# Kernel tuning notes

Hardware: AMD Instinct MI355X
Metric: run time of the kernel (lower is better)

## Reference

```python
import jax, jax.numpy as jnp
import numpy as np

HID = 2048      # hidden_size
H = 16          # num_heads == num_kv_heads (stack in fwd forces MHA)
DH = HID // H   # head_size = 128
QKV = 3 * H * DH  # 6144
THETA = 10000.0
EPS = 1e-5      # flash-attn RMSNorm default eps
B, L = 4, 2048


def setup_inputs() -> dict:
    key = jax.random.key(0)
    k1, k2, k3 = jax.random.split(key, 3)
    hidden_states = jax.random.normal(k1, (B, L, HID), dtype=jnp.float32)
    # weights stored as (in, out); scaled like a typical init so activations stay sane
    W_qkvg = jax.random.normal(k2, (HID, QKV + HID), dtype=jnp.float32) * 0.02
    W_out = jax.random.normal(k3, (HID, HID), dtype=jnp.float32) * 0.02
    return {"hidden_states": hidden_states, "W_qkvg": W_qkvg, "W_out": W_out}


def _rmsnorm(x):
    # elementwise_affine=False: pure rms normalization over head dim
    return x * jax.lax.rsqrt(jnp.mean(x * x, axis=-1, keepdims=True) + EPS)


def _rope(x, seqlen_offset=0):
    # x: (B, L, H, DH), non-interleaved (GPT-NeoX style rotate-half)
    half = DH // 2
    inv_freq = 1.0 / (THETA ** (jnp.arange(half, dtype=jnp.float32) * 2.0 / DH))
    pos = jnp.arange(seqlen_offset, seqlen_offset + x.shape[1], dtype=jnp.float32)
    ang = pos[:, None] * inv_freq[None, :]                  # (L, half)
    cos = jnp.cos(ang)[None, :, None, :]                    # (1,L,1,half)
    sin = jnp.sin(ang)[None, :, None, :]
    x1, x2 = x[..., :half], x[..., half:]
    return jnp.concatenate([x1 * cos - x2 * sin, x1 * sin + x2 * cos], axis=-1)


def _attention_forward(hidden_states, W_qkvg, W_out):
    b, l, _ = hidden_states.shape
    proj = hidden_states @ W_qkvg                           # (B,L,QKV+HID)
    qkv_flat, gate = proj[..., :QKV], proj[..., QKV:]
    gate = jax.nn.sigmoid(gate)
    qkv = qkv_flat.reshape(b, l, 3 * H, DH)
    q, k, v = qkv[:, :, :H], qkv[:, :, H:2 * H], qkv[:, :, 2 * H:]
    q = _rope(_rmsnorm(q))
    k = _rope(_rmsnorm(k))
    # causal softmax attention (math of flash_attn_func)
    scores = jnp.einsum('blhd,bmhd->bhlm', q, k) / np.sqrt(DH).astype(np.float32)
    causal = jnp.tril(jnp.ones((l, l), dtype=bool))
    scores = jnp.where(causal[None, None], scores, jnp.finfo(scores.dtype).min)
    attn = jax.nn.softmax(scores, axis=-1)
    out = jnp.einsum('bhlm,bmhd->blhd', attn, v).reshape(b, l, HID)
    out = out * gate
    return out @ W_out


def reference(hidden_states, W_qkvg, W_out):
    return _attention_forward(hidden_states, W_qkvg, W_out)
```

## Files before the change

### kernel.cpp

```cpp
#include <hip/hip_runtime.h>


typedef __attribute__((ext_vector_type(8))) short bf16x8;
typedef __attribute__((ext_vector_type(4))) float f32x4;
typedef __attribute__((ext_vector_type(4))) unsigned short us4;

#if __has_builtin(__builtin_amdgcn_exp2f)
#define EXP2(x) __builtin_amdgcn_exp2f(x)
#else
#define EXP2(x) exp2f(x)
#endif

__device__ __forceinline__ unsigned short f2bf(float f) {
    unsigned int x = __float_as_uint(f);
    unsigned int r = x + 0x7fffu + ((x >> 16) & 1u);
    return (unsigned short)(r >> 16);
}
__device__ __forceinline__ unsigned short f2bf_fast(float f) {
    return (unsigned short)((__float_as_uint(f) + 0x8000u) >> 16);
}
__device__ __forceinline__ float bf2f(unsigned short u) {
    return __uint_as_float(((unsigned int)u) << 16);
}

__device__ __forceinline__ void gll16(const unsigned short* g, unsigned short* l) {
    __builtin_amdgcn_global_load_lds(
        (const __attribute__((address_space(1))) unsigned int*)g,
        (__attribute__((address_space(3))) unsigned int*)l, 16, 0, 0);
}

__global__ __launch_bounds__(256) void cvt_bf16(const float* __restrict__ in,
                                                unsigned short* __restrict__ out) {
    int i = blockIdx.x * 256 + threadIdx.x;
    float4 v = ((const float4*)in)[i];
    us4 r;
    r[0] = f2bf(v.x); r[1] = f2bf(v.y); r[2] = f2bf(v.z); r[3] = f2bf(v.w);
    ((us4*)out)[i] = r;
}

__global__ __launch_bounds__(256) void transpose_cvt(const float* __restrict__ in,
                                                     unsigned short* __restrict__ out,
                                                     int R, int C) {
    __shared__ float t[32][33];
    int c0 = blockIdx.x * 32, r0 = blockIdx.y * 32;
    int tx = threadIdx.x, ty = threadIdx.y;
#pragma unroll
    for (int i = 0; i < 4; i++)
        t[ty + i * 8][tx] = in[(size_t)(r0 + ty + i * 8) * C + c0 + tx];
    __syncthreads();
#pragma unroll
    for (int i = 0; i < 4; i++)
        out[(size_t)(c0 + ty + i * 8) * R + r0 + tx] = f2bf(t[tx][ty + i * 8]);
}

__device__ __forceinline__ void gemm_core(const unsigned short* __restrict__ A,
                                          const unsigned short* __restrict__ Bt,
                                          int K, int rowA0, int colB0,
                                          unsigned short* As, unsigned short* Bs,
                                          f32x4 acc[4][4]) {
    const int tid = threadIdx.x;
    const int w = tid >> 6, lane = tid & 63;
    const int quad = lane >> 4, l15 = lane & 15;
    const int wm = w >> 1, wn = w & 1;
    const int lr = lane >> 3;
    const int lc = ((lane & 7) ^ lr) * 8;

    const unsigned short* ga[4]; const unsigned short* gb[4];
    unsigned short* la[4]; unsigned short* lb[4];
#pragma unroll
    for (int i = 0; i < 4; i++) {
        int r = w * 32 + i * 8;
        ga[i] = A  + (size_t)(rowA0 + r + lr) * K + lc;
        gb[i] = Bt + (size_t)(colB0 + r + lr) * K + lc;
        la[i] = As + r * 64;
        lb[i] = Bs + r * 64;
    }
    const int sw = (l15 & 7);
    const int KT = K >> 6;
    for (int kt = 0; kt < KT; kt++) {
        const int ko = kt * 64;
#pragma unroll
        for (int i = 0; i < 4; i++) gll16(ga[i] + ko, la[i]);
#pragma unroll
        for (int i = 0; i < 4; i++) gll16(gb[i] + ko, lb[i]);
        __syncthreads();
#pragma unroll
        for (int kk = 0; kk < 2; kk++) {
            bf16x8 af[4], bfr[4];
#pragma unroll
            for (int mi = 0; mi < 4; mi++)
                af[mi] = *(const bf16x8*)&As[(wm * 64 + mi * 16 + l15) * 64 +
                                             (((kk * 4 + quad) ^ sw) * 8)];
#pragma unroll
            for (int ni = 0; ni < 4; ni++)
                bfr[ni] = *(const bf16x8*)&Bs[(wn * 64 + ni * 16 + l15) * 64 +
                                              (((kk * 4 + quad) ^ sw) * 8)];
#pragma unroll
            for (int mi = 0; mi < 4; mi++)
#pragma unroll
                for (int ni = 0; ni < 4; ni++)
                    acc[mi][ni] = __builtin_amdgcn_mfma_f32_16x16x32_bf16(
                        af[mi], bfr[ni], acc[mi][ni], 0, 0, 0);
        }
        __syncthreads();
    }
}

__global__ __launch_bounds__(256) void gemm_qkvg(const unsigned short* __restrict__ A,
                                                 const unsigned short* __restrict__ Bt,
                                                 unsigned short* __restrict__ Qb,
                                                 unsigned short* __restrict__ Kb,
                                                 unsigned short* __restrict__ Vt,
                                                 unsigned short* __restrict__ Gb) {
    __shared__ unsigned short smem[128 * 128];
    unsigned short* As = smem;
    unsigned short* Bs = smem + 128 * 64;
    f32x4 acc[4][4];
    f32x4 z = {0.f, 0.f, 0.f, 0.f};
#pragma unroll
    for (int i = 0; i < 4; i++)
#pragma unroll
        for (int j = 0; j < 4; j++) acc[i][j] = z;

    const int rowA0 = blockIdx.y * 128, colB0 = blockIdx.x * 128;
    gemm_core(A, Bt, 2048, rowA0, colB0, As, Bs, acc);

    const int tid = threadIdx.x, w = tid >> 6, lane = tid & 63;
    const int quad = lane >> 4, l15 = lane & 15;
    const int wm = w >> 1, wn = w & 1;
    const int sec = blockIdx.x >> 4;
    const int h = blockIdx.x & 15;

    if (sec == 2) {
        __syncthreads();
#pragma unroll
        for (int mi = 0; mi < 4; mi++)
#pragma unroll
            for (int ni = 0; ni < 4; ni++)
#pragma unroll
                for (int i = 0; i < 4; i++) {
                    int ll = wm * 64 + mi * 16 + quad * 4 + i;
                    int d  = wn * 64 + ni * 16 + l15;
                    smem[d * 128 + (((ll >> 3) ^ (d & 15)) * 8) + (ll & 7)] =
                        f2bf(acc[mi][ni][i]);
                }
        __syncthreads();
        const int b_ = rowA0 >> 11, l0 = rowA0 & 2047;
        const int r = tid >> 1, hf = tid & 1;
        unsigned short* drow = Vt + (size_t)(b_ * 16 + h) * 128 * 2048 +
                               (size_t)r * 2048 + l0;
#pragma unroll
        for (int jj = 0; jj < 8; jj++) {
            int jcol = hf * 8 + jj;
            *(bf16x8*)(drow + jcol * 8) =
                *(const bf16x8*)&smem[r * 128 + ((jcol ^ (r & 15)) * 8)];
        }
    } else if (sec == 3) {
#pragma unroll
        for (int mi = 0; mi < 4; mi++)
#pragma unroll
            for (int ni = 0; ni < 4; ni++)
#pragma unroll
                for (int i = 0; i < 4; i++) {
                    int rowg = rowA0 + wm * 64 + mi * 16 + quad * 4 + i;
                    int d = wn * 64 + ni * 16 + l15;
                    float g = 1.f / (1.f + __expf(-acc[mi][ni][i]));
                    Gb[((size_t)rowg << 11) + h * 128 + d] = f2bf(g);
                }
    } else {
        unsigned short* dst = (sec == 0) ? Qb : Kb;
#pragma unroll
        for (int mi = 0; mi < 4; mi++)
#pragma unroll
            for (int ni = 0; ni < 4; ni++)
#pragma unroll
                for (int i = 0; i < 4; i++) {
                    int rowg = rowA0 + wm * 64 + mi * 16 + quad * 4 + i;
                    int d = wn * 64 + ni * 16 + l15;
                    int b_ = rowg >> 11, l_ = rowg & 2047;
                    dst[(((size_t)(b_ * 16 + h) * 2048 + l_) << 7) + d] =
                        f2bf(acc[mi][ni][i]);
                }
    }
}

__global__ __launch_bounds__(256) void gemm_out(const unsigned short* __restrict__ A,
                                                const unsigned short* __restrict__ Bt,
                                                float* __restrict__ C) {
    __shared__ unsigned short As[128 * 64], Bs[128 * 64];
    f32x4 acc[4][4];
    f32x4 z = {0.f, 0.f, 0.f, 0.f};
#pragma unroll
    for (int i = 0; i < 4; i++)
#pragma unroll
        for (int j = 0; j < 4; j++) acc[i][j] = z;

    const int rowA0 = blockIdx.y * 128, colB0 = blockIdx.x * 128;
    gemm_core(A, Bt, 2048, rowA0, colB0, As, Bs, acc);

    const int tid = threadIdx.x, w = tid >> 6, lane = tid & 63;
    const int quad = lane >> 4, l15 = lane & 15;
    const int wm = w >> 1, wn = w & 1;
#pragma unroll
    for (int mi = 0; mi < 4; mi++)
#pragma unroll
        for (int ni = 0; ni < 4; ni++)
#pragma unroll
            for (int i = 0; i < 4; i++) {
                int rowg = rowA0 + wm * 64 + mi * 16 + quad * 4 + i;
                int col = colB0 + wn * 64 + ni * 16 + l15;
                C[(size_t)rowg * 2048 + col] = acc[mi][ni][i];
            }
}

__global__ __launch_bounds__(256) void rmsnorm_rope(unsigned short* __restrict__ Qp,
                                                    unsigned short* __restrict__ Kp) {
    unsigned short* X = blockIdx.y ? Kp : Qp;
    const int tid = threadIdx.x;
    const int row = blockIdx.x * 4 + (tid >> 6);
    const int lane = tid & 63;
    unsigned short* p = X + (size_t)row * 128;
    const int l_ = row & 2047;
    float x1 = bf2f(p[lane]);
    float x2 = bf2f(p[lane + 64]);
    float ss = x1 * x1 + x2 * x2;
#pragma unroll
    for (int off = 32; off >= 1; off >>= 1) ss += __shfl_xor(ss, off, 64);
    float r = rsqrtf(ss * (1.f / 128.f) + 1e-5f);
    x1 *= r; x2 *= r;
    float inv = exp2f(-(float)lane * (13.287712379549449f / 64.f));
    float ang = (float)l_ * inv;
    float sn, cs;
    sincosf(ang, &sn, &cs);
    p[lane]      = f2bf(x1 * cs - x2 * sn);
    p[lane + 64] = f2bf(x1 * sn + x2 * cs);
}

__global__ __launch_bounds__(512) void fa_kernel(const unsigned short* __restrict__ Q,
                                                 const unsigned short* __restrict__ K,
                                                 const unsigned short* __restrict__ Vt,
                                                 const unsigned short* __restrict__ G,
                                                 unsigned short* __restrict__ Og) {
    __shared__ unsigned short Ks[64 * 128];
    __shared__ unsigned short Vs[128 * 64];
    __shared__ unsigned short Ps[256 * 32];
    const int g = blockIdx.x;
    const int bh = (g & 7) | ((g >> 6) << 3);
    const int qc = (g >> 3) & 7;
    const int tid = threadIdx.x, w = tid >> 6, lane = tid & 63;
    const int quad = lane >> 4, l15 = lane & 15;
    const int sw = l15 & 7;
    const int qrow0 = qc * 256 + w * 32;
    const float CS = 0.12751740395609812f;

    bf16x8 qf[2][4];
#pragma unroll
    for (int mi = 0; mi < 2; mi++)
#pragma unroll
        for (int kt = 0; kt < 4; kt++)
            qf[mi][kt] = *(const bf16x8*)(Q + ((size_t)bh * 2048 + qrow0 + mi * 16 + l15) * 128
                                             + kt * 32 + quad * 8);

    f32x4 o[2][8];
    f32x4 z = {0.f, 0.f, 0.f, 0.f};
#pragma unroll
    for (int mi = 0; mi < 2; mi++)
#pragma unroll
        for (int nj = 0; nj < 8; nj++) o[mi][nj] = z;
    float rowsum[2][4];
#pragma unroll
    for (int mi = 0; mi < 2; mi++)
#pragma unroll
        for (int i = 0; i < 4; i++) rowsum[mi][i] = 0.f;

    const unsigned short* Kbase = K + (size_t)bh * 2048 * 128;
    const unsigned short* Vtb   = Vt + (size_t)bh * 128 * 2048;

    const int pr0 = w * 32 + l15, pr1 = pr0 + 16;
    const int pk0 = (pr0 >> 1) & 3, pk1 = (pr1 >> 1) & 3;

    const int NJ = 4 * (qc + 1);
    for (int j = 0; j < NJ; j++) {
        __syncthreads();

        {
            const int rowoff = lane >> 4, c = lane & 15;
#pragma unroll
            for (int i = 0; i < 2; i++) {
                int r0 = w * 8 + i * 4;
                int row = r0 + rowoff;
                int cs_ = (c & 8) | ((c & 7) ^ (row & 7));
                gll16(Kbase + (size_t)(j * 64 + row) * 128 + cs_ * 8, Ks + r0 * 128);
            }
        }
        {
            const int rowoff = lane >> 3, c = lane & 7;
#pragma unroll
            for (int i = 0; i < 2; i++) {
                int r0 = w * 16 + i * 8;
                int row = r0 + rowoff;
                gll16(Vtb + (size_t)row * 2048 + j * 64 + ((c ^ (row & 7)) * 8),
                      Vs + r0 * 64);
            }
        }
        __syncthreads();

        if (j * 64 >= qrow0 + 32) continue;

        f32x4 s[2][4];
#pragma unroll
        for (int mi = 0; mi < 2; mi++)
#pragma unroll
            for (int nj = 0; nj < 4; nj++) s[mi][nj] = z;
#pragma unroll
        for (int kt = 0; kt < 4; kt++)
#pragma unroll
            for (int nj = 0; nj < 4; nj++) {
                bf16x8 bfr = *(const bf16x8*)&Ks[(nj * 16 + l15) * 128 +
                                                 (((kt * 4 + quad) ^ sw) * 8)];
                s[0][nj] = __builtin_amdgcn_mfma_f32_16x16x32_bf16(qf[0][kt], bfr, s[0][nj], 0, 0, 0);
                s[1][nj] = __builtin_amdgcn_mfma_f32_16x16x32_bf16(qf[1][kt], bfr, s[1][nj], 0, 0, 0);
            }

        const bool diag = (j * 64 + 63 > qrow0);
#pragma unroll
        for (int hh = 0; hh < 2; hh++) {
#pragma unroll
            for (int mi = 0; mi < 2; mi++)
#pragma unroll
                for (int njh = 0; njh < 2; njh++) {
                    const int nj = hh * 2 + njh;
#pragma unroll
                    for (int i = 0; i < 4; i++) {
                        float pp = EXP2(s[mi][nj][i] * CS);
                        int row_l = mi * 16 + quad * 4 + i;
                        if (diag) {
                            int col_g = j * 64 + nj * 16 + l15;
                            if (col_g > qrow0 + row_l) pp = 0.f;
                        }
                        rowsum[mi][i] += pp;
                        int row = w * 32 + row_l;
                        int kv = njh * 16 + l15;
                        Ps[row * 32 + ((((kv >> 3) ^ ((row >> 1) & 3)) * 8)) + (kv & 7)] =
                            f2bf_fast(pp);
                    }
                }
            bf16x8 a0 = *(const bf16x8*)&Ps[pr0 * 32 + ((quad ^ pk0) * 8)];
            bf16x8 a1 = *(const bf16x8*)&Ps[pr1 * 32 + ((quad ^ pk1) * 8)];
#pragma unroll
            for (int nj = 0; nj < 8; nj++) {
                bf16x8 bfr = *(const bf16x8*)&Vs[(nj * 16 + l15) * 64 +
                                                 (((hh * 4 + quad) ^ sw) * 8)];
                o[0][nj] = __builtin_amdgcn_mfma_f32_16x16x32_bf16(a0, bfr, o[0][nj], 0, 0, 0);
                o[1][nj] = __builtin_amdgcn_mfma_f32_16x16x32_bf16(a1, bfr, o[1][nj], 0, 0, 0);
            }
        }
    }

    const int b_ = bh >> 4, h = bh & 15;
#pragma unroll
    for (int mi = 0; mi < 2; mi++)
#pragma unroll
        for (int i = 0; i < 4; i++) {
            float t = rowsum[mi][i];
#pragma unroll
            for (int off = 1; off < 16; off <<= 1) t += __shfl_xor(t, off, 16);
            float rl = 1.f / t;
            int l_ = qrow0 + mi * 16 + quad * 4 + i;
#pragma unroll
            for (int nj = 0; nj < 8; nj++) {
                int d = nj * 16 + l15;
                size_t gi = ((size_t)(b_ * 2048 + l_) * 2048) + h * 128 + d;
                Og[gi] = f2bf(o[mi][nj][i] * rl * bf2f(G[gi]));
            }
        }
}

extern "C" void kernel_launch(void* const* d_in, const int* in_sizes, int n_in,
                              void* d_out, int out_size, void* d_ws, size_t ws_size,
                              hipStream_t stream) {
    const float* X  = (const float*)d_in[0];
    const float* Wq = (const float*)d_in[1];
    const float* Wo = (const float*)d_in[2];
    float* out = (float*)d_out;

    char* ws = (char*)d_ws;
    const size_t SZ = 33554432ull;
    unsigned short* Xb  = (unsigned short*)(ws);
    unsigned short* Wqt = (unsigned short*)(ws + SZ);
    unsigned short* Wot = (unsigned short*)(ws + 2 * SZ);
    unsigned short* Qb  = (unsigned short*)(ws + 2 * SZ + 8388608ull);
    unsigned short* Kb  = (unsigned short*)(ws + 3 * SZ + 8388608ull);
    unsigned short* Vt  = (unsigned short*)(ws + 4 * SZ + 8388608ull);
    unsigned short* Gb  = (unsigned short*)(ws + 5 * SZ + 8388608ull);
    unsigned short* OG  = Xb;

    cvt_bf16<<<16384, 256, 0, stream>>>(X, Xb);
    transpose_cvt<<<dim3(256, 64), dim3(32, 8), 0, stream>>>(Wq, Wqt, 2048, 8192);
    transpose_cvt<<<dim3(64, 64),  dim3(32, 8), 0, stream>>>(Wo, Wot, 2048, 2048);

    gemm_qkvg<<<dim3(64, 64), 256, 0, stream>>>(Xb, Wqt, Qb, Kb, Vt, Gb);

    rmsnorm_rope<<<dim3(32768, 2), 256, 0, stream>>>(Qb, Kb);

    fa_kernel<<<512, 512, 0, stream>>>(Qb, Kb, Vt, Gb, OG);

    gemm_out<<<dim3(16, 64), 256, 0, stream>>>(OG, Wot, out);
}
```

Before: 774.8 us.

## Rewrite projection GEMMs as 256x256 double-buffered pipelined tiles with block swizzle

Replaces the 128x128 single-buffered GEMM core with a 256x256 tile computed by 512 threads (8 waves). Global-to-LDS loads for the next two k-steps are staged in quarter-sized pieces between MFMA phases, using explicit vmcnt waits, raw barriers and setprio. Block indices are remapped so neighbouring blocks share operand tiles in cache. The goal is to hide load latency and raise per-block data reuse in both GEMMs, at the cost of 128KB LDS per block, higher register pressure and fewer blocks in flight.

```diff
diff --git a/kernel.cpp b/kernel.cpp
--- a/kernel.cpp
+++ b/kernel.cpp
@@ -28,6 +28,15 @@
         (const __attribute__((address_space(1))) unsigned int*)g,
         (__attribute__((address_space(3))) unsigned int*)l, 16, 0, 0);
 }
+
+__device__ __forceinline__ void barx() {
+    asm volatile("" ::: "memory");
+    __builtin_amdgcn_s_barrier();
+    asm volatile("" ::: "memory");
+}
+#define LGKM0() asm volatile("s_waitcnt lgkmcnt(0)" ::: "memory")
+#define VM6()   asm volatile("s_waitcnt vmcnt(6)" ::: "memory")
+#define VM0()   asm volatile("s_waitcnt vmcnt(0)" ::: "memory")
 
 __global__ __launch_bounds__(256) void cvt_bf16(const float* __restrict__ in,
                                                 unsigned short* __restrict__ out) {
@@ -53,163 +62,200 @@
         out[(size_t)(c0 + ty + i * 8) * R + r0 + tx] = f2bf(t[tx][ty + i * 8]);
 }
 
-__device__ __forceinline__ void gemm_core(const unsigned short* __restrict__ A,
-                                          const unsigned short* __restrict__ Bt,
-                                          int K, int rowA0, int colB0,
-                                          unsigned short* As, unsigned short* Bs,
-                                          f32x4 acc[4][4]) {
+__device__ __forceinline__ void gemm256_core(const unsigned short* __restrict__ A,
+                                             const unsigned short* __restrict__ Bt,
+                                             int K, int rowA0, int colB0,
+                                             unsigned short* sm,
+                                             f32x4 acc[8][4]) {
     const int tid = threadIdx.x;
     const int w = tid >> 6, lane = tid & 63;
     const int quad = lane >> 4, l15 = lane & 15;
-    const int wm = w >> 1, wn = w & 1;
+    const int wm = w >> 2, wn = w & 3;
     const int lr = lane >> 3;
     const int lc = ((lane & 7) ^ lr) * 8;
-
-    const unsigned short* ga[4]; const unsigned short* gb[4];
-    unsigned short* la[4]; unsigned short* lb[4];
-#pragma unroll
-    for (int i = 0; i < 4; i++) {
-        int r = w * 32 + i * 8;
-        ga[i] = A  + (size_t)(rowA0 + r + lr) * K + lc;
-        gb[i] = Bt + (size_t)(colB0 + r + lr) * K + lc;
-        la[i] = As + r * 64;
-        lb[i] = Bs + r * 64;
+    const int NT = K >> 6;
+
+    const unsigned short* pA = A  + (size_t)(rowA0 + w * 16 + lr) * K + lc;
+    const unsigned short* pB = Bt + (size_t)(colB0 + w * 16 + lr) * K + lc;
+    unsigned short* lw = sm + w * 16 * 64;
+
+#define STAGE(tt, isB, h)                                                       \
+    do {                                                                        \
+        const unsigned short* gp_ = ((isB) ? pB : pA) +                         \
+            (size_t)(h) * 128 * K + (size_t)(tt) * 64;                          \
+        unsigned short* lp_ = lw + (((tt) & 1) * 4 + (isB) * 2 + (h)) * 8192;   \
+        gll16(gp_, lp_);                                                        \
+        gll16(gp_ + (size_t)8 * K, lp_ + 8 * 64);                               \
+    } while (0)
+
+    STAGE(0, 1, 0); STAGE(0, 1, 1); STAGE(0, 0, 0); STAGE(0, 0, 1);
+    STAGE(1, 1, 0); STAGE(1, 1, 1); STAGE(1, 0, 0);
+    VM6();
+    barx();
+
+    for (int t = 0; t < NT; ++t) {
+        const unsigned short* Asl = sm + ((t & 1) * 4 + wm) * 8192;
+        const unsigned short* Bsl = sm + ((t & 1) * 4 + 2 + (wn >> 1)) * 8192;
+        bf16x8 bfrag[4][2];
+#pragma unroll
+        for (int q = 0; q < 4; ++q) {
+            if (q == 0) {
+#pragma unroll
+                for (int nj = 0; nj < 4; ++nj)
+#pragma unroll
+                    for (int kk = 0; kk < 2; ++kk) {
+                        int r = (wn & 1) * 64 + nj * 16 + l15;
+                        bfrag[nj][kk] = *(const bf16x8*)&Bsl[r * 64 +
+                            (((kk * 4 + quad) ^ (r & 7)) * 8)];
+                    }
+            }
+            bf16x8 afr[2][2];
+#pragma unroll
+            for (int mi = 0; mi < 2; ++mi)
+#pragma unroll
+                for (int kk = 0; kk < 2; ++kk) {
+                    int r = q * 32 + mi * 16 + l15;
+                    afr[mi][kk] = *(const bf16x8*)&Asl[r * 64 +
+                        (((kk * 4 + quad) ^ (r & 7)) * 8)];
+                }
+            if (q == 0)      { if (t + 1 < NT) STAGE(t + 1, 0, 1); }
+            else if (q == 1) { if (t + 2 < NT) STAGE(t + 2, 1, 0); }
+            else if (q == 2) { if (t + 2 < NT) STAGE(t + 2, 1, 1); }
+            else {
+                if (t + 2 < NT)      { STAGE(t + 2, 0, 0); VM6(); }
+                else if (t + 1 < NT) { VM0(); }
+            }
+            barx();
+            LGKM0();
+            __builtin_amdgcn_s_setprio(1);
+#pragma unroll
+            for (int mi = 0; mi < 2; ++mi)
+#pragma unroll
+                for (int nj = 0; nj < 4; ++nj)
+#pragma unroll
+                    for (int kk = 0; kk < 2; ++kk)
+                        acc[q * 2 + mi][nj] = __builtin_amdgcn_mfma_f32_16x16x32_bf16(
+                            afr[mi][kk], bfrag[nj][kk], acc[q * 2 + mi][nj], 0, 0, 0);
+            __builtin_amdgcn_s_setprio(0);
+            barx();
+        }
     }
-    const int sw = (l15 & 7);
-    const int KT = K >> 6;
-    for (int kt = 0; kt < KT; kt++) {
-        const int ko = kt * 64;
-#pragma unroll
-        for (int i = 0; i < 4; i++) gll16(ga[i] + ko, la[i]);
-#pragma unroll
-        for (int i = 0; i < 4; i++) gll16(gb[i] + ko, lb[i]);
-        __syncthreads();
-#pragma unroll
-        for (int kk = 0; kk < 2; kk++) {
-            bf16x8 af[4], bfr[4];
-#pragma unroll
-            for (int mi = 0; mi < 4; mi++)
-                af[mi] = *(const bf16x8*)&As[(wm * 64 + mi * 16 + l15) * 64 +
-                                             (((kk * 4 + quad) ^ sw) * 8)];
-#pragma unroll
-            for (int ni = 0; ni < 4; ni++)
-                bfr[ni] = *(const bf16x8*)&Bs[(wn * 64 + ni * 16 + l15) * 64 +
-                                              (((kk * 4 + quad) ^ sw) * 8)];
-#pragma unroll
-            for (int mi = 0; mi < 4; mi++)
-#pragma unroll
-                for (int ni = 0; ni < 4; ni++)
-                    acc[mi][ni] = __builtin_amdgcn_mfma_f32_16x16x32_bf16(
-                        af[mi], bfr[ni], acc[mi][ni], 0, 0, 0);
-        }
-        __syncthreads();
-    }
-}
-
-__global__ __launch_bounds__(256) void gemm_qkvg(const unsigned short* __restrict__ A,
+#undef STAGE
+}
+
+__global__ __launch_bounds__(512) void gemm_qkvg(const unsigned short* __restrict__ A,
                                                  const unsigned short* __restrict__ Bt,
                                                  unsigned short* __restrict__ Qb,
                                                  unsigned short* __restrict__ Kb,
                                                  unsigned short* __restrict__ Vt,
                                                  unsigned short* __restrict__ Gb) {
-    __shared__ unsigned short smem[128 * 128];
-    unsigned short* As = smem;
-    unsigned short* Bs = smem + 128 * 64;
-    f32x4 acc[4][4];
+    __shared__ unsigned short sm[8 * 8192];
+    f32x4 acc[8][4];
     f32x4 z = {0.f, 0.f, 0.f, 0.f};
 #pragma unroll
-    for (int i = 0; i < 4; i++)
+    for (int i = 0; i < 8; i++)
 #pragma unroll
         for (int j = 0; j < 4; j++) acc[i][j] = z;
 
-    const int rowA0 = blockIdx.y * 128, colB0 = blockIdx.x * 128;
-    gemm_core(A, Bt, 2048, rowA0, colB0, As, Bs, acc);
+    const int g = blockIdx.y * 32 + blockIdx.x;
+    const int gs = (g & 7) * 128 + (g >> 3);
+    const int bx = gs & 31, by = gs >> 5;
+    const int rowA0 = by * 256, colB0 = bx * 256;
+    gemm256_core(A, Bt, 2048, rowA0, colB0, sm, acc);
 
     const int tid = threadIdx.x, w = tid >> 6, lane = tid & 63;
     const int quad = lane >> 4, l15 = lane & 15;
-    const int wm = w >> 1, wn = w & 1;
-    const int sec = blockIdx.x >> 4;
-    const int h = blockIdx.x & 15;
+    const int wm = w >> 2, wn = w & 3;
+    const int sec = colB0 >> 11;
+    const int hbase = (colB0 & 2047) >> 7;
 
     if (sec == 2) {
-        __syncthreads();
-#pragma unroll
-        for (int mi = 0; mi < 4; mi++)
-#pragma unroll
-            for (int ni = 0; ni < 4; ni++)
-#pragma unroll
-                for (int i = 0; i < 4; i++) {
-                    int ll = wm * 64 + mi * 16 + quad * 4 + i;
-                    int d  = wn * 64 + ni * 16 + l15;
-                    smem[d * 128 + (((ll >> 3) ^ (d & 15)) * 8) + (ll & 7)] =
-                        f2bf(acc[mi][ni][i]);
+#pragma unroll
+        for (int mi = 0; mi < 8; ++mi)
+#pragma unroll
+            for (int nj = 0; nj < 4; ++nj)
+#pragma unroll
+                for (int i = 0; i < 4; ++i) {
+                    int ll = wm * 128 + mi * 16 + quad * 4 + i;
+                    int c  = wn * 64 + nj * 16 + l15;
+                    int hh = c >> 7, d = c & 127;
+                    sm[hh * 32768 + d * 256 + (((ll >> 3) ^ (d & 31)) * 8) + (ll & 7)] =
+                        f2bf(acc[mi][nj][i]);
                 }
         __syncthreads();
         const int b_ = rowA0 >> 11, l0 = rowA0 & 2047;
-        const int r = tid >> 1, hf = tid & 1;
-        unsigned short* drow = Vt + (size_t)(b_ * 16 + h) * 128 * 2048 +
-                               (size_t)r * 2048 + l0;
-#pragma unroll
-        for (int jj = 0; jj < 8; jj++) {
-            int jcol = hf * 8 + jj;
-            *(bf16x8*)(drow + jcol * 8) =
-                *(const bf16x8*)&smem[r * 128 + ((jcol ^ (r & 15)) * 8)];
+        const int d = tid >> 2, part = tid & 3;
+#pragma unroll
+        for (int hh = 0; hh < 2; ++hh) {
+            unsigned short* drow = Vt +
+                ((size_t)(b_ * 16 + hbase + hh) * 128 + d) * 2048 + l0 + part * 64;
+#pragma unroll
+            for (int j = 0; j < 8; ++j) {
+                int chunk = part * 8 + j;
+                *(bf16x8*)(drow + j * 8) =
+                    *(const bf16x8*)&sm[hh * 32768 + d * 256 + ((chunk ^ (d & 31)) * 8)];
+            }
         }
     } else if (sec == 3) {
 #pragma unroll
-        for (int mi = 0; mi < 4; mi++)
-#pragma unroll
-            for (int ni = 0; ni < 4; ni++)
-#pragma unroll
-                for (int i = 0; i < 4; i++) {
-                    int rowg = rowA0 + wm * 64 + mi * 16 + quad * 4 + i;
-                    int d = wn * 64 + ni * 16 + l15;
-                    float g = 1.f / (1.f + __expf(-acc[mi][ni][i]));
-                    Gb[((size_t)rowg << 11) + h * 128 + d] = f2bf(g);
+        for (int mi = 0; mi < 8; ++mi)
+#pragma unroll
+            for (int nj = 0; nj < 4; ++nj)
+#pragma unroll
+                for (int i = 0; i < 4; ++i) {
+                    int rowg = rowA0 + wm * 128 + mi * 16 + quad * 4 + i;
+                    int c = wn * 64 + nj * 16 + l15;
+                    int h = hbase + (c >> 7), d = c & 127;
+                    float gv = 1.f / (1.f + __expf(-acc[mi][nj][i]));
+                    Gb[((size_t)rowg << 11) + h * 128 + d] = f2bf(gv);
                 }
     } else {
         unsigned short* dst = (sec == 0) ? Qb : Kb;
 #pragma unroll
-        for (int mi = 0; mi < 4; mi++)
-#pragma unroll
-            for (int ni = 0; ni < 4; ni++)
-#pragma unroll
-                for (int i = 0; i < 4; i++) {
-                    int rowg = rowA0 + wm * 64 + mi * 16 + quad * 4 + i;
-                    int d = wn * 64 + ni * 16 + l15;
+        for (int mi = 0; mi < 8; ++mi)
+#pragma unroll
+            for (int nj = 0; nj < 4; ++nj)
+#pragma unroll
+                for (int i = 0; i < 4; ++i) {
+                    int rowg = rowA0 + wm * 128 + mi * 16 + quad * 4 + i;
+                    int c = wn * 64 + nj * 16 + l15;
+                    int h = hbase + (c >> 7), d = c & 127;
                     int b_ = rowg >> 11, l_ = rowg & 2047;
                     dst[(((size_t)(b_ * 16 + h) * 2048 + l_) << 7) + d] =
-                        f2bf(acc[mi][ni][i]);
+                        f2bf(acc[mi][nj][i]);
                 }
     }
 }
 
-__global__ __launch_bounds__(256) void gemm_out(const unsigned short* __restrict__ A,
+__global__ __launch_bounds__(512) void gemm_out(const unsigned short* __restrict__ A,
                                                 const unsigned short* __restrict__ Bt,
                                                 float* __restrict__ C) {
-    __shared__ unsigned short As[128 * 64], Bs[128 * 64];
-    f32x4 acc[4][4];
+    __shared__ unsigned short sm[8 * 8192];
+    f32x4 acc[8][4];
     f32x4 z = {0.f, 0.f, 0.f, 0.f};
 #pragma unroll
-    for (int i = 0; i < 4; i++)
+    for (int i = 0; i < 8; i++)
 #pragma unroll
         for (int j = 0; j < 4; j++) acc[i][j] = z;
 
-    const int rowA0 = blockIdx.y * 128, colB0 = blockIdx.x * 128;
-    gemm_core(A, Bt, 2048, rowA0, colB0, As, Bs, acc);
+    const int g = blockIdx.y * 8 + blockIdx.x;
+    const int gs = (g & 7) * 32 + (g >> 3);
+    const int bx = gs & 7, by = gs >> 3;
+    const int rowA0 = by * 256, colB0 = bx * 256;
+    gemm256_core(A, Bt, 2048, rowA0, colB0, sm, acc);
 
     const int tid = threadIdx.x, w = tid >> 6, lane = tid & 63;
     const int quad = lane >> 4, l15 = lane & 15;
-    const int wm = w >> 1, wn = w & 1;
-#pragma unroll
-    for (int mi = 0; mi < 4; mi++)
-#pragma unroll
-        for (int ni = 0; ni < 4; ni++)
-#pragma unroll
-            for (int i = 0; i < 4; i++) {
-                int rowg = rowA0 + wm * 64 + mi * 16 + quad * 4 + i;
-                int col = colB0 + wn * 64 + ni * 16 + l15;
-                C[(size_t)rowg * 2048 + col] = acc[mi][ni][i];
+    const int wm = w >> 2, wn = w & 3;
+#pragma unroll
+    for (int mi = 0; mi < 8; ++mi)
+#pragma unroll
+        for (int nj = 0; nj < 4; ++nj)
+#pragma unroll
+            for (int i = 0; i < 4; ++i) {
+                int rowg = rowA0 + wm * 128 + mi * 16 + quad * 4 + i;
+                int col = colB0 + wn * 64 + nj * 16 + l15;
+                C[(size_t)rowg * 2048 + col] = acc[mi][nj][i];
             }
 }
 
@@ -399,11 +445,11 @@
     transpose_cvt<<<dim3(256, 64), dim3(32, 8), 0, stream>>>(Wq, Wqt, 2048, 8192);
     transpose_cvt<<<dim3(64, 64),  dim3(32, 8), 0, stream>>>(Wo, Wot, 2048, 2048);
 
-    gemm_qkvg<<<dim3(64, 64), 256, 0, stream>>>(Xb, Wqt, Qb, Kb, Vt, Gb);
+    gemm_qkvg<<<dim3(32, 32), 512, 0, stream>>>(Xb, Wqt, Qb, Kb, Vt, Gb);
 
     rmsnorm_rope<<<dim3(32768, 2), 256, 0, stream>>>(Qb, Kb);
 
     fa_kernel<<<512, 512, 0, stream>>>(Qb, Kb, Vt, Gb, OG);
 
-    gemm_out<<<dim3(16, 64), 256, 0, stream>>>(OG, Wot, out);
-}
+    gemm_out<<<dim3(8, 32), 512, 0, stream>>>(OG, Wot, out);
+}
```

Measured after the change: 702.7 us. 1.1x faster.
